# Kernel optimization log

Measured on AMD Instinct MI355X. Metric: run time of the kernel, lower is better.

The kernel has to match this reference:

```python
import jax, jax.numpy as jnp
import numpy as np

N_NODES = 10000
N_EDGES = 160000
HIDDEN = 256
HEADS = 8
LN_EPS = 1e-5


def setup_inputs() -> dict:
    key = jax.random.key(0)
    ks = jax.random.split(key, 8)
    s = 1.0 / np.sqrt(HIDDEN)
    return {
        "node_embeddings": jax.random.normal(ks[0], (1, N_NODES, HIDDEN), jnp.float32),
        "edge_index": jax.random.randint(ks[1], (2, N_EDGES), 0, N_NODES, dtype=jnp.int32),
        "Wq": jax.random.normal(ks[2], (HIDDEN, HIDDEN), jnp.float32) * s,
        "Wk": jax.random.normal(ks[3], (HIDDEN, HIDDEN), jnp.float32) * s,
        "Wv": jax.random.normal(ks[4], (HIDDEN, HIDDEN), jnp.float32) * s,
        "Wo": jax.random.normal(ks[5], (HIDDEN, HIDDEN), jnp.float32) * s,
        "ln_gamma": jnp.ones((HIDDEN,), jnp.float32),
        "ln_beta": jnp.zeros((HIDDEN,), jnp.float32),
    }


def reference(node_embeddings, edge_index, Wq, Wk, Wv, Wo, ln_gamma, ln_beta):
    B, N, Dm = node_embeddings.shape
    H = HEADS
    hd = Dm // H
    scale = 1.0 / np.sqrt(hd)

    def heads(x):  # [B,N,Dm] -> [B,H,N,hd]
        return x.reshape(B, N, H, hd).transpose(0, 2, 1, 3)

    Q = heads(node_embeddings @ Wq)
    K = heads(node_embeddings @ Wk)
    V = heads(node_embeddings @ Wv)

    src, dst = edge_index[0], edge_index[1]
    Qe = Q[:, :, src, :]           # [B,H,E,hd]
    Ke = K[:, :, dst, :]
    Ve = V[:, :, dst, :]

    scores = jnp.einsum('bhed,bhed->bhe', Qe, Ke) * scale   # [B,H,E]
    s_t = scores.transpose(2, 0, 1)                          # [E,B,H]
    smax = jax.ops.segment_max(s_t, src, num_segments=N)    # [N,B,H]
    ex = jnp.exp(s_t - smax[src])                            # [E,B,H]
    denom = jax.ops.segment_sum(ex, src, num_segments=N)    # [N,B,H]
    attn = ex / denom[src]                                   # scatter-softmax weights

    wV = attn[..., None] * Ve.transpose(2, 0, 1, 3)          # [E,B,H,hd]
    agg = jax.ops.segment_sum(wV, src, num_segments=N)      # [N,B,H,hd]
    attn_out = agg.transpose(1, 0, 2, 3).reshape(B, N, Dm)   # [B,N,Dm]

    out = attn_out @ Wo
    x = out + node_embeddings
    mu = jnp.mean(x, axis=-1, keepdims=True)
    var = jnp.mean((x - mu) ** 2, axis=-1, keepdims=True)
    return (x - mu) * jax.lax.rsqrt(var + LN_EPS) * ln_gamma + ln_beta
```

## Files before the change

kernel.cpp:

```cpp
#include <hip/hip_runtime.h>

#define NN 10000
#define NE 160000
#define DM 256
#define CAP 96
#define LN_EPSF 1e-5f
#define SCALEF 0.17677669529663687f

typedef unsigned short u16;
typedef __attribute__((ext_vector_type(4))) u16 u16x4;
typedef __attribute__((ext_vector_type(8))) u16 u16x8;
typedef __attribute__((ext_vector_type(4))) float f32x4;
typedef __attribute__((ext_vector_type(8))) short short8;

__device__ __forceinline__ float b2f(u16 u) { return __uint_as_float(((unsigned)u) << 16); }
__device__ __forceinline__ u16 f2b(float f) {
    unsigned u = __float_as_uint(f);
    return (u16)((u + 0x7fffu + ((u >> 16) & 1u)) >> 16);
}
__device__ __forceinline__ int clampi(int v) { return v < 0 ? 0 : (v >= NN ? NN - 1 : v); }

__global__ void k_fill_zero_f32(float* __restrict__ o, int n) {
    int i = blockIdx.x * 256 + threadIdx.x;
    if (i < n) o[i] = 0.f;
}

__global__ void k_prep(const float* __restrict__ Wq, const float* __restrict__ Wk,
                       const float* __restrict__ Wv, const float* __restrict__ Wo,
                       u16* __restrict__ Wt, int* __restrict__ cnt) {
    int id = blockIdx.x * 256 + threadIdx.x;
    if (id < NN) cnt[id] = 0;
    int m = id >> 16;
    int rc = id & 65535;
    int r = rc >> 8, c = rc & 255;
    const float* W = (m == 0) ? Wq : (m == 1) ? Wk : (m == 2) ? Wv : Wo;
    Wt[m * 65536 + c * 256 + r] = f2b(W[r * 256 + c]);
}

__global__ __launch_bounds__(256) void k_qkv_bucket(const float* __restrict__ X, const u16* __restrict__ Wt,
                                                    u16* __restrict__ Q, u16* __restrict__ KV,
                                                    const int* __restrict__ EI, int* __restrict__ cnt,
                                                    int* __restrict__ buck) {
    constexpr int AS = 40;
    __shared__ u16 At[64 * AS];
    __shared__ u16 Bt[256 * AS];
    if (blockIdx.y == 3) {
        int e = blockIdx.x * 256 + threadIdx.x;
        if (e < NE) {
            int s = clampi(EI[e]);
            int slot = atomicAdd(&cnt[s], 1);
            if (slot < CAP) buck[s * CAP + slot] = clampi(EI[NE + e]);
        }
        return;
    }
    if (blockIdx.x >= 157) return;
    const int t = threadIdx.x;
    const int w = t >> 6, l = t & 63, quad = l >> 4, m16 = l & 15;
    const int mat = blockIdx.y;
    const u16* Wm = Wt + mat * 65536;
    const int node0 = blockIdx.x * 64;
    f32x4 acc[4][4];
#pragma unroll
    for (int i = 0; i < 4; i++)
#pragma unroll
        for (int j = 0; j < 4; j++) acc[i][j] = (f32x4){0.f, 0.f, 0.f, 0.f};
    const int arow = t >> 2, ac8 = (t & 3) * 8;
    for (int k0 = 0; k0 < DM; k0 += 32) {
        u16x8 av = {0, 0, 0, 0, 0, 0, 0, 0};
        int anode = node0 + arow;
        if (anode < NN) {
            const float* xp = X + (size_t)anode * DM + k0 + ac8;
            f32x4 a0 = *(const f32x4*)(xp);
            f32x4 a1 = *(const f32x4*)(xp + 4);
            av[0] = f2b(a0[0]); av[1] = f2b(a0[1]); av[2] = f2b(a0[2]); av[3] = f2b(a0[3]);
            av[4] = f2b(a1[0]); av[5] = f2b(a1[1]); av[6] = f2b(a1[2]); av[7] = f2b(a1[3]);
        }
        *(u16x8*)(At + arow * AS + ac8) = av;
        const u16* bsrc = Wm + t * DM + k0;
        u16x8 b0 = *(const u16x8*)(bsrc);
        u16x8 b1 = *(const u16x8*)(bsrc + 8);
        u16x8 b2 = *(const u16x8*)(bsrc + 16);
        u16x8 b3 = *(const u16x8*)(bsrc + 24);
        u16* bd = Bt + t * AS;
        *(u16x8*)(bd) = b0;
        *(u16x8*)(bd + 8) = b1;
        *(u16x8*)(bd + 16) = b2;
        *(u16x8*)(bd + 24) = b3;
        __syncthreads();
        short8 a[4], b[4];
#pragma unroll
        for (int rt = 0; rt < 4; rt++)
            a[rt] = *(const short8*)(At + (rt * 16 + m16) * AS + quad * 8);
#pragma unroll
        for (int ct = 0; ct < 4; ct++)
            b[ct] = *(const short8*)(Bt + (w * 64 + ct * 16 + m16) * AS + quad * 8);
#pragma unroll
        for (int rt = 0; rt < 4; rt++)
#pragma unroll
            for (int ct = 0; ct < 4; ct++)
                acc[rt][ct] = __builtin_amdgcn_mfma_f32_16x16x32_bf16(a[rt], b[ct], acc[rt][ct], 0, 0, 0);
        __syncthreads();
    }
#pragma unroll
    for (int rt = 0; rt < 4; rt++) {
#pragma unroll
        for (int ct = 0; ct < 4; ct++) {
            int col = w * 64 + ct * 16 + m16;
#pragma unroll
            for (int r = 0; r < 4; r++) {
                int node = node0 + rt * 16 + quad * 4 + r;
                if (node < NN) {
                    u16 v = f2b(acc[rt][ct][r]);
                    if (mat == 0) Q[(size_t)node * DM + col] = v;
                    else KV[(size_t)node * 512 + (col >> 2) * 8 + (col & 3) + ((mat == 2) ? 4 : 0)] = v;
                }
            }
        }
    }
}

#define UPD(mm, ss, AA, kv, p) do {                  \
    float nm_ = fmaxf(mm, p);                        \
    float al_ = __expf(mm - nm_);                    \
    float pe_ = __expf(p - nm_);                     \
    ss = ss * al_ + pe_;                             \
    AA[0] = AA[0] * al_ + pe_ * b2f(kv[4]);          \
    AA[1] = AA[1] * al_ + pe_ * b2f(kv[5]);          \
    AA[2] = AA[2] * al_ + pe_ * b2f(kv[6]);          \
    AA[3] = AA[3] * al_ + pe_ * b2f(kv[7]);          \
    mm = nm_;                                        \
} while (0)

__global__ __launch_bounds__(256) void k_edge(const u16* __restrict__ Q, const u16* __restrict__ KV,
                                              const int* __restrict__ cnt, const int* __restrict__ buck,
                                              u16* __restrict__ attn) {
    const int t = threadIdx.x;
    const int w = t >> 6, l = t & 63;
    const int node = blockIdx.x * 4 + w;
    const int d0 = l * 4;
    int deg = cnt[node];
    if (deg > CAP) deg = CAP;
    const int* bl = buck + node * CAP;
    u16x4 q4 = *(const u16x4*)(Q + (size_t)node * DM + d0);
    float qf0 = b2f(q4[0]) * SCALEF, qf1 = b2f(q4[1]) * SCALEF;
    float qf2 = b2f(q4[2]) * SCALEF, qf3 = b2f(q4[3]) * SCALEF;
    float m0 = -3.0e38f, m1 = -3.0e38f, m2 = -3.0e38f, m3 = -3.0e38f;
    float s0 = 0.f, s1 = 0.f, s2 = 0.f, s3 = 0.f;
    f32x4 A0 = {0.f, 0.f, 0.f, 0.f}, A1 = {0.f, 0.f, 0.f, 0.f};
    f32x4 A2 = {0.f, 0.f, 0.f, 0.f}, A3 = {0.f, 0.f, 0.f, 0.f};
    int i = 0;
    int deg4 = deg & ~3;
    for (; i < deg4; i += 4) {
        int4 e4 = *(const int4*)(bl + i);
        u16x8 kv0 = *(const u16x8*)(KV + (size_t)e4.x * 512 + l * 8);
        u16x8 kv1 = *(const u16x8*)(KV + (size_t)e4.y * 512 + l * 8);
        u16x8 kv2 = *(const u16x8*)(KV + (size_t)e4.z * 512 + l * 8);
        u16x8 kv3 = *(const u16x8*)(KV + (size_t)e4.w * 512 + l * 8);
        float p0 = qf0 * b2f(kv0[0]) + qf1 * b2f(kv0[1]) + qf2 * b2f(kv0[2]) + qf3 * b2f(kv0[3]);
        float p1 = qf0 * b2f(kv1[0]) + qf1 * b2f(kv1[1]) + qf2 * b2f(kv1[2]) + qf3 * b2f(kv1[3]);
        float p2 = qf0 * b2f(kv2[0]) + qf1 * b2f(kv2[1]) + qf2 * b2f(kv2[2]) + qf3 * b2f(kv2[3]);
        float p3 = qf0 * b2f(kv3[0]) + qf1 * b2f(kv3[1]) + qf2 * b2f(kv3[2]) + qf3 * b2f(kv3[3]);
        p0 += __shfl_xor(p0, 1, 64); p1 += __shfl_xor(p1, 1, 64);
        p2 += __shfl_xor(p2, 1, 64); p3 += __shfl_xor(p3, 1, 64);
        p0 += __shfl_xor(p0, 2, 64); p1 += __shfl_xor(p1, 2, 64);
        p2 += __shfl_xor(p2, 2, 64); p3 += __shfl_xor(p3, 2, 64);
        p0 += __shfl_xor(p0, 4, 64); p1 += __shfl_xor(p1, 4, 64);
        p2 += __shfl_xor(p2, 4, 64); p3 += __shfl_xor(p3, 4, 64);
        UPD(m0, s0, A0, kv0, p0);
        UPD(m1, s1, A1, kv1, p1);
        UPD(m2, s2, A2, kv2, p2);
        UPD(m3, s3, A3, kv3, p3);
    }
    for (; i < deg; ++i) {
        int dst = bl[i];
        u16x8 kv = *(const u16x8*)(KV + (size_t)dst * 512 + l * 8);
        float p = qf0 * b2f(kv[0]) + qf1 * b2f(kv[1]) + qf2 * b2f(kv[2]) + qf3 * b2f(kv[3]);
        p += __shfl_xor(p, 1, 64);
        p += __shfl_xor(p, 2, 64);
        p += __shfl_xor(p, 4, 64);
        UPD(m0, s0, A0, kv, p);
    }
    float nm = fmaxf(fmaxf(m0, m1), fmaxf(m2, m3));
    float w0 = __expf(m0 - nm), w1 = __expf(m1 - nm);
    float w2 = __expf(m2 - nm), w3 = __expf(m3 - nm);
    float s = s0 * w0 + s1 * w1 + s2 * w2 + s3 * w3;
    float inv = (s > 0.f) ? 1.f / s : 0.f;
    u16x4 o;
    o[0] = f2b((A0[0] * w0 + A1[0] * w1 + A2[0] * w2 + A3[0] * w3) * inv);
    o[1] = f2b((A0[1] * w0 + A1[1] * w1 + A2[1] * w2 + A3[1] * w3) * inv);
    o[2] = f2b((A0[2] * w0 + A1[2] * w1 + A2[2] * w2 + A3[2] * w3) * inv);
    o[3] = f2b((A0[3] * w0 + A1[3] * w1 + A2[3] * w2 + A3[3] * w3) * inv);
    *(u16x4*)(attn + (size_t)node * DM + d0) = o;
}

__global__ __launch_bounds__(256) void k_gemm_out_ln(const u16* __restrict__ In, const u16* __restrict__ WoT,
                                                     const float* __restrict__ X, const float* __restrict__ g,
                                                     const float* __restrict__ b, float* __restrict__ out) {
    constexpr int AS = 40;
    __shared__ u16 At[64 * AS];
    __shared__ u16 Bt[256 * AS];
    __shared__ float gbuf[256], bbuf[256];
    __shared__ float redS[4][64], redQ[4][64];
    __shared__ float muS[64], rsS[64];
    const int t = threadIdx.x;
    gbuf[t] = g[t];
    bbuf[t] = b[t];
    const int w = t >> 6, l = t & 63, quad = l >> 4, m16 = l & 15;
    const int node0 = blockIdx.x * 64;
    f32x4 acc[4][4];
#pragma unroll
    for (int i = 0; i < 4; i++)
#pragma unroll
        for (int j = 0; j < 4; j++) acc[i][j] = (f32x4){0.f, 0.f, 0.f, 0.f};
    const int arow = t >> 2, ac8 = (t & 3) * 8;
    for (int k0 = 0; k0 < DM; k0 += 32) {
        u16x8 av = {0, 0, 0, 0, 0, 0, 0, 0};
        int anode = node0 + arow;
        if (anode < NN) av = *(const u16x8*)(In + (size_t)anode * DM + k0 + ac8);
        *(u16x8*)(At + arow * AS + ac8) = av;
        const u16* bsrc = WoT + t * DM + k0;
        u16x8 b0 = *(const u16x8*)(bsrc);
        u16x8 b1 = *(const u16x8*)(bsrc + 8);
        u16x8 b2 = *(const u16x8*)(bsrc + 16);
        u16x8 b3 = *(const u16x8*)(bsrc + 24);
        u16* bd = Bt + t * AS;
        *(u16x8*)(bd) = b0;
        *(u16x8*)(bd + 8) = b1;
        *(u16x8*)(bd + 16) = b2;
        *(u16x8*)(bd + 24) = b3;
        __syncthreads();
        short8 a[4], bf[4];
#pragma unroll
        for (int rt = 0; rt < 4; rt++)
            a[rt] = *(const short8*)(At + (rt * 16 + m16) * AS + quad * 8);
#pragma unroll
        for (int ct = 0; ct < 4; ct++)
            bf[ct] = *(const short8*)(Bt + (w * 64 + ct * 16 + m16) * AS + quad * 8);
#pragma unroll
        for (int rt = 0; rt < 4; rt++)
#pragma unroll
            for (int ct = 0; ct < 4; ct++)
                acc[rt][ct] = __builtin_amdgcn_mfma_f32_16x16x32_bf16(a[rt], bf[ct], acc[rt][ct], 0, 0, 0);
        __syncthreads();
    }
#pragma unroll
    for (int rt = 0; rt < 4; rt++)
#pragma unroll
        for (int ct = 0; ct < 4; ct++) {
            int col = w * 64 + ct * 16 + m16;
#pragma unroll
            for (int r = 0; r < 4; r++) {
                int node = node0 + rt * 16 + quad * 4 + r;
                float x = (node < NN) ? X[(size_t)node * DM + col] : 0.f;
                acc[rt][ct][r] += x;
            }
        }
#pragma unroll
    for (int rt = 0; rt < 4; rt++) {
#pragma unroll
        for (int r = 0; r < 4; r++) {
            float p1 = acc[rt][0][r] + acc[rt][1][r] + acc[rt][2][r] + acc[rt][3][r];
            float p2 = acc[rt][0][r] * acc[rt][0][r] + acc[rt][1][r] * acc[rt][1][r] +
                       acc[rt][2][r] * acc[rt][2][r] + acc[rt][3][r] * acc[rt][3][r];
#pragma unroll
            for (int o = 1; o < 16; o <<= 1) {
                p1 += __shfl_xor(p1, o, 64);
                p2 += __shfl_xor(p2, o, 64);
            }
            if (m16 == 0) {
                int row = rt * 16 + quad * 4 + r;
                redS[w][row] = p1;
                redQ[w][row] = p2;
            }
        }
    }
    __syncthreads();
    if (t < 64) {
        float s1t = redS[0][t] + redS[1][t] + redS[2][t] + redS[3][t];
        float s2t = redQ[0][t] + redQ[1][t] + redQ[2][t] + redQ[3][t];
        float mm = s1t * (1.f / DM);
        float var = s2t * (1.f / DM) - mm * mm;
        muS[t] = mm;
        rsS[t] = rsqrtf(var + LN_EPSF);
    }
    __syncthreads();
#pragma unroll
    for (int rt = 0; rt < 4; rt++)
#pragma unroll
        for (int ct = 0; ct < 4; ct++) {
            int col = w * 64 + ct * 16 + m16;
#pragma unroll
            for (int r = 0; r < 4; r++) {
                int row = rt * 16 + quad * 4 + r;
                int node = node0 + row;
                if (node < NN)
                    out[(size_t)node * DM + col] = (acc[rt][ct][r] - muS[row]) * rsS[row] * gbuf[col] + bbuf[col];
            }
        }
}

extern "C" void kernel_launch(void* const* d_in, const int* in_sizes, int n_in,
                              void* d_out, int out_size, void* d_ws, size_t ws_size,
                              hipStream_t stream) {
    (void)in_sizes; (void)n_in;
    const float* X  = (const float*)d_in[0];
    const int*   EI = (const int*)d_in[1];
    const float* Wq = (const float*)d_in[2];
    const float* Wk = (const float*)d_in[3];
    const float* Wv = (const float*)d_in[4];
    const float* Wo = (const float*)d_in[5];
    const float* g  = (const float*)d_in[6];
    const float* be = (const float*)d_in[7];

    const size_t SWT  = (size_t)4 * 65536 * 2;
    const size_t SKV  = (size_t)NN * 512 * 2;
    const size_t SAT  = (size_t)NN * DM * 2;
    const size_t SCNT = (size_t)NN * 4;
    const size_t SBK  = (size_t)NN * CAP * 4;
    const size_t need = SWT + SKV + SAT + SCNT + SBK;
    if (ws_size < need) {
        k_fill_zero_f32<<<(out_size + 255) / 256, 256, 0, stream>>>((float*)d_out, out_size);
        return;
    }
    char* p = (char*)d_ws;
    u16* Wt   = (u16*)p; p += SWT;
    u16* KVb  = (u16*)p; p += SKV;
    u16* attn = (u16*)p; p += SAT;
    int* cnt  = (int*)p; p += SCNT;
    int* buck = (int*)p; p += SBK;
    u16* Qb = (u16*)d_out;

    k_prep<<<1024, 256, 0, stream>>>(Wq, Wk, Wv, Wo, Wt, cnt);
    k_qkv_bucket<<<dim3(625, 4), 256, 0, stream>>>(X, Wt, Qb, KVb, EI, cnt, buck);
    k_edge<<<NN / 4, 256, 0, stream>>>(Qb, KVb, cnt, buck, attn);
    k_gemm_out_ln<<<157, 256, 0, stream>>>(attn, Wt + 3 * 65536, X, g, be, (float*)d_out);
}
```

Measured before the change: 143.7 us.

## Fuse all four stages into one cooperative persistent kernel with grid syncs

Replaces the four separate launches (weight prep, QKV GEMM plus edge bucketing, edge attention, output GEMM plus LayerNorm) with a single cooperative kernel of 512 blocks. Grid-wide syncs separate the phases, and each phase walks its work items in a grid-stride loop. The aim is to remove launch gaps and inter-kernel drain and fill. In exchange, the edge phase runs with fewer resident blocks, grid syncs cost time, and the output GEMM phase uses only 157 of 512 blocks. If the cooperative launch fails, the old four-kernel path runs instead.

```diff
diff --git a/kernel.cpp b/kernel.cpp
--- a/kernel.cpp
+++ b/kernel.cpp
@@ -1,4 +1,7 @@
 #include <hip/hip_runtime.h>
+#include <hip/hip_cooperative_groups.h>
+
+namespace cg = cooperative_groups;
 
 #define NN 10000
 #define NE 160000
@@ -6,6 +9,7 @@
 #define CAP 96
 #define LN_EPSF 1e-5f
 #define SCALEF 0.17677669529663687f
+#define GRIDB 512
 
 typedef unsigned short u16;
 typedef __attribute__((ext_vector_type(4))) u16 u16x4;
@@ -24,6 +28,18 @@
     int i = blockIdx.x * 256 + threadIdx.x;
     if (i < n) o[i] = 0.f;
 }
+
+#define UPD(mm, ss, AA, kv, p) do {                  \
+    float nm_ = fmaxf(mm, p);                        \
+    float al_ = __expf(mm - nm_);                    \
+    float pe_ = __expf(p - nm_);                     \
+    ss = ss * al_ + pe_;                             \
+    AA[0] = AA[0] * al_ + pe_ * b2f(kv[4]);          \
+    AA[1] = AA[1] * al_ + pe_ * b2f(kv[5]);          \
+    AA[2] = AA[2] * al_ + pe_ * b2f(kv[6]);          \
+    AA[3] = AA[3] * al_ + pe_ * b2f(kv[7]);          \
+    mm = nm_;                                        \
+} while (0)
 
 __global__ void k_prep(const float* __restrict__ Wq, const float* __restrict__ Wk,
                        const float* __restrict__ Wv, const float* __restrict__ Wo,
@@ -118,18 +134,6 @@
         }
     }
 }
-
-#define UPD(mm, ss, AA, kv, p) do {                  \
-    float nm_ = fmaxf(mm, p);                        \
-    float al_ = __expf(mm - nm_);                    \
-    float pe_ = __expf(p - nm_);                     \
-    ss = ss * al_ + pe_;                             \
-    AA[0] = AA[0] * al_ + pe_ * b2f(kv[4]);          \
-    AA[1] = AA[1] * al_ + pe_ * b2f(kv[5]);          \
-    AA[2] = AA[2] * al_ + pe_ * b2f(kv[6]);          \
-    AA[3] = AA[3] * al_ + pe_ * b2f(kv[7]);          \
-    mm = nm_;                                        \
-} while (0)
 
 __global__ __launch_bounds__(256) void k_edge(const u16* __restrict__ Q, const u16* __restrict__ KV,
                                               const int* __restrict__ cnt, const int* __restrict__ buck,
@@ -299,6 +303,272 @@
         }
 }
 
+__global__ __launch_bounds__(256, 2) void k_fused(
+    const float* __restrict__ X, const int* __restrict__ EI,
+    const float* __restrict__ Wq, const float* __restrict__ Wk,
+    const float* __restrict__ Wv, const float* __restrict__ Wo,
+    const float* __restrict__ g, const float* __restrict__ be,
+    float* out, u16* __restrict__ Wt, u16* __restrict__ KV,
+    u16* __restrict__ attn, int* __restrict__ cnt, int* __restrict__ buck,
+    u16* Q) {
+    constexpr int AS = 40;
+    __shared__ u16 At[64 * AS];
+    __shared__ u16 Bt[256 * AS];
+    __shared__ float gbuf[256], bbuf[256];
+    __shared__ float redS[4][64], redQ[4][64], muS[64], rsS[64];
+
+    const int t = threadIdx.x;
+    const int bid = blockIdx.x;
+    const int w = t >> 6, l = t & 63, quad = l >> 4, m16 = l & 15;
+    cg::grid_group gg = cg::this_grid();
+
+    for (int id = bid * 256 + t; id < 262144; id += GRIDB * 256) {
+        if (id < NN) cnt[id] = 0;
+        int m = id >> 16;
+        int rc = id & 65535;
+        int r = rc >> 8, c = rc & 255;
+        const float* W = (m == 0) ? Wq : (m == 1) ? Wk : (m == 2) ? Wv : Wo;
+        Wt[m * 65536 + c * 256 + r] = f2b(W[r * 256 + c]);
+    }
+    __threadfence();
+    gg.sync();
+
+    for (int item = bid; item < 1096; item += GRIDB) {
+        if (item >= 471) {
+            int e = (item - 471) * 256 + t;
+            if (e < NE) {
+                int s = clampi(EI[e]);
+                int slot = atomicAdd(&cnt[s], 1);
+                if (slot < CAP) buck[s * CAP + slot] = clampi(EI[NE + e]);
+            }
+            continue;
+        }
+        const int mat = item / 157;
+        const int tx = item % 157;
+        const u16* Wm = Wt + mat * 65536;
+        const int node0 = tx * 64;
+        f32x4 acc[4][4];
+#pragma unroll
+        for (int i = 0; i < 4; i++)
+#pragma unroll
+            for (int j = 0; j < 4; j++) acc[i][j] = (f32x4){0.f, 0.f, 0.f, 0.f};
+        const int arow = t >> 2, ac8 = (t & 3) * 8;
+        for (int k0 = 0; k0 < DM; k0 += 32) {
+            u16x8 av = {0, 0, 0, 0, 0, 0, 0, 0};
+            int anode = node0 + arow;
+            if (anode < NN) {
+                const float* xp = X + (size_t)anode * DM + k0 + ac8;
+                f32x4 a0 = *(const f32x4*)(xp);
+                f32x4 a1 = *(const f32x4*)(xp + 4);
+                av[0] = f2b(a0[0]); av[1] = f2b(a0[1]); av[2] = f2b(a0[2]); av[3] = f2b(a0[3]);
+                av[4] = f2b(a1[0]); av[5] = f2b(a1[1]); av[6] = f2b(a1[2]); av[7] = f2b(a1[3]);
+            }
+            *(u16x8*)(At + arow * AS + ac8) = av;
+            const u16* bsrc = Wm + t * DM + k0;
+            u16x8 b0 = *(const u16x8*)(bsrc);
+            u16x8 b1 = *(const u16x8*)(bsrc + 8);
+            u16x8 b2 = *(const u16x8*)(bsrc + 16);
+            u16x8 b3 = *(const u16x8*)(bsrc + 24);
+            u16* bd = Bt + t * AS;
+            *(u16x8*)(bd) = b0;
+            *(u16x8*)(bd + 8) = b1;
+            *(u16x8*)(bd + 16) = b2;
+            *(u16x8*)(bd + 24) = b3;
+            __syncthreads();
+            short8 a[4], b[4];
+#pragma unroll
+            for (int rt = 0; rt < 4; rt++)
+                a[rt] = *(const short8*)(At + (rt * 16 + m16) * AS + quad * 8);
+#pragma unroll
+            for (int ct = 0; ct < 4; ct++)
+                b[ct] = *(const short8*)(Bt + (w * 64 + ct * 16 + m16) * AS + quad * 8);
+#pragma unroll
+            for (int rt = 0; rt < 4; rt++)
+#pragma unroll
+                for (int ct = 0; ct < 4; ct++)
+                    acc[rt][ct] = __builtin_amdgcn_mfma_f32_16x16x32_bf16(a[rt], b[ct], acc[rt][ct], 0, 0, 0);
+            __syncthreads();
+        }
+#pragma unroll
+        for (int rt = 0; rt < 4; rt++) {
+#pragma unroll
+            for (int ct = 0; ct < 4; ct++) {
+                int col = w * 64 + ct * 16 + m16;
+#pragma unroll
+                for (int r = 0; r < 4; r++) {
+                    int node = node0 + rt * 16 + quad * 4 + r;
+                    if (node < NN) {
+                        u16 v = f2b(acc[rt][ct][r]);
+                        if (mat == 0) Q[(size_t)node * DM + col] = v;
+                        else KV[(size_t)node * 512 + (col >> 2) * 8 + (col & 3) + ((mat == 2) ? 4 : 0)] = v;
+                    }
+                }
+            }
+        }
+    }
+    __threadfence();
+    gg.sync();
+
+    {
+        const int d0 = l * 4;
+        for (int it = bid; it < 2500; it += GRIDB) {
+            const int node = it * 4 + w;
+            int deg = cnt[node];
+            if (deg > CAP) deg = CAP;
+            const int* bl = buck + node * CAP;
+            u16x4 q4 = *(const u16x4*)(Q + (size_t)node * DM + d0);
+            float qf0 = b2f(q4[0]) * SCALEF, qf1 = b2f(q4[1]) * SCALEF;
+            float qf2 = b2f(q4[2]) * SCALEF, qf3 = b2f(q4[3]) * SCALEF;
+            float m0 = -3.0e38f, m1 = -3.0e38f, m2 = -3.0e38f, m3 = -3.0e38f;
+            float s0 = 0.f, s1 = 0.f, s2 = 0.f, s3 = 0.f;
+            f32x4 A0 = {0.f, 0.f, 0.f, 0.f}, A1 = {0.f, 0.f, 0.f, 0.f};
+            f32x4 A2 = {0.f, 0.f, 0.f, 0.f}, A3 = {0.f, 0.f, 0.f, 0.f};
+            int i = 0;
+            int deg4 = deg & ~3;
+            for (; i < deg4; i += 4) {
+                int4 e4 = *(const int4*)(bl + i);
+                u16x8 kv0 = *(const u16x8*)(KV + (size_t)e4.x * 512 + l * 8);
+                u16x8 kv1 = *(const u16x8*)(KV + (size_t)e4.y * 512 + l * 8);
+                u16x8 kv2 = *(const u16x8*)(KV + (size_t)e4.z * 512 + l * 8);
+                u16x8 kv3 = *(const u16x8*)(KV + (size_t)e4.w * 512 + l * 8);
+                float p0 = qf0 * b2f(kv0[0]) + qf1 * b2f(kv0[1]) + qf2 * b2f(kv0[2]) + qf3 * b2f(kv0[3]);
+                float p1 = qf0 * b2f(kv1[0]) + qf1 * b2f(kv1[1]) + qf2 * b2f(kv1[2]) + qf3 * b2f(kv1[3]);
+                float p2 = qf0 * b2f(kv2[0]) + qf1 * b2f(kv2[1]) + qf2 * b2f(kv2[2]) + qf3 * b2f(kv2[3]);
+                float p3 = qf0 * b2f(kv3[0]) + qf1 * b2f(kv3[1]) + qf2 * b2f(kv3[2]) + qf3 * b2f(kv3[3]);
+                p0 += __shfl_xor(p0, 1, 64); p1 += __shfl_xor(p1, 1, 64);
+                p2 += __shfl_xor(p2, 1, 64); p3 += __shfl_xor(p3, 1, 64);
+                p0 += __shfl_xor(p0, 2, 64); p1 += __shfl_xor(p1, 2, 64);
+                p2 += __shfl_xor(p2, 2, 64); p3 += __shfl_xor(p3, 2, 64);
+                p0 += __shfl_xor(p0, 4, 64); p1 += __shfl_xor(p1, 4, 64);
+                p2 += __shfl_xor(p2, 4, 64); p3 += __shfl_xor(p3, 4, 64);
+                UPD(m0, s0, A0, kv0, p0);
+                UPD(m1, s1, A1, kv1, p1);
+                UPD(m2, s2, A2, kv2, p2);
+                UPD(m3, s3, A3, kv3, p3);
+            }
+            for (; i < deg; ++i) {
+                int dst = bl[i];
+                u16x8 kv = *(const u16x8*)(KV + (size_t)dst * 512 + l * 8);
+                float p = qf0 * b2f(kv[0]) + qf1 * b2f(kv[1]) + qf2 * b2f(kv[2]) + qf3 * b2f(kv[3]);
+                p += __shfl_xor(p, 1, 64);
+                p += __shfl_xor(p, 2, 64);
+                p += __shfl_xor(p, 4, 64);
+                UPD(m0, s0, A0, kv, p);
+            }
+            float nm = fmaxf(fmaxf(m0, m1), fmaxf(m2, m3));
+            float w0 = __expf(m0 - nm), w1 = __expf(m1 - nm);
+            float w2 = __expf(m2 - nm), w3 = __expf(m3 - nm);
+            float S = s0 * w0 + s1 * w1 + s2 * w2 + s3 * w3;
+            float inv = (S > 0.f) ? 1.f / S : 0.f;
+            u16x4 o;
+            o[0] = f2b((A0[0] * w0 + A1[0] * w1 + A2[0] * w2 + A3[0] * w3) * inv);
+            o[1] = f2b((A0[1] * w0 + A1[1] * w1 + A2[1] * w2 + A3[1] * w3) * inv);
+            o[2] = f2b((A0[2] * w0 + A1[2] * w1 + A2[2] * w2 + A3[2] * w3) * inv);
+            o[3] = f2b((A0[3] * w0 + A1[3] * w1 + A2[3] * w2 + A3[3] * w3) * inv);
+            *(u16x4*)(attn + (size_t)node * DM + d0) = o;
+        }
+    }
+    __threadfence();
+    gg.sync();
+
+    for (int it = bid; it < 157; it += GRIDB) {
+        const u16* WoT = Wt + 3 * 65536;
+        gbuf[t] = g[t];
+        bbuf[t] = be[t];
+        const int node0 = it * 64;
+        f32x4 acc[4][4];
+#pragma unroll
+        for (int i = 0; i < 4; i++)
+#pragma unroll
+            for (int j = 0; j < 4; j++) acc[i][j] = (f32x4){0.f, 0.f, 0.f, 0.f};
+        const int arow = t >> 2, ac8 = (t & 3) * 8;
+        for (int k0 = 0; k0 < DM; k0 += 32) {
+            u16x8 av = {0, 0, 0, 0, 0, 0, 0, 0};
+            int anode = node0 + arow;
+            if (anode < NN) av = *(const u16x8*)(attn + (size_t)anode * DM + k0 + ac8);
+            *(u16x8*)(At + arow * AS + ac8) = av;
+            const u16* bsrc = WoT + t * DM + k0;
+            u16x8 b0 = *(const u16x8*)(bsrc);
+            u16x8 b1 = *(const u16x8*)(bsrc + 8);
+            u16x8 b2 = *(const u16x8*)(bsrc + 16);
+            u16x8 b3 = *(const u16x8*)(bsrc + 24);
+            u16* bd = Bt + t * AS;
+            *(u16x8*)(bd) = b0;
+            *(u16x8*)(bd + 8) = b1;
+            *(u16x8*)(bd + 16) = b2;
+            *(u16x8*)(bd + 24) = b3;
+            __syncthreads();
+            short8 a[4], bf[4];
+#pragma unroll
+            for (int rt = 0; rt < 4; rt++)
+                a[rt] = *(const short8*)(At + (rt * 16 + m16) * AS + quad * 8);
+#pragma unroll
+            for (int ct = 0; ct < 4; ct++)
+                bf[ct] = *(const short8*)(Bt + (w * 64 + ct * 16 + m16) * AS + quad * 8);
+#pragma unroll
+            for (int rt = 0; rt < 4; rt++)
+#pragma unroll
+                for (int ct = 0; ct < 4; ct++)
+                    acc[rt][ct] = __builtin_amdgcn_mfma_f32_16x16x32_bf16(a[rt], bf[ct], acc[rt][ct], 0, 0, 0);
+            __syncthreads();
+        }
+#pragma unroll
+        for (int rt = 0; rt < 4; rt++)
+#pragma unroll
+            for (int ct = 0; ct < 4; ct++) {
+                int col = w * 64 + ct * 16 + m16;
+#pragma unroll
+                for (int r = 0; r < 4; r++) {
+                    int node = node0 + rt * 16 + quad * 4 + r;
+                    float x = (node < NN) ? X[(size_t)node * DM + col] : 0.f;
+                    acc[rt][ct][r] += x;
+                }
+            }
+#pragma unroll
+        for (int rt = 0; rt < 4; rt++) {
+#pragma unroll
+            for (int r = 0; r < 4; r++) {
+                float p1 = acc[rt][0][r] + acc[rt][1][r] + acc[rt][2][r] + acc[rt][3][r];
+                float p2 = acc[rt][0][r] * acc[rt][0][r] + acc[rt][1][r] * acc[rt][1][r] +
+                           acc[rt][2][r] * acc[rt][2][r] + acc[rt][3][r] * acc[rt][3][r];
+#pragma unroll
+                for (int o = 1; o < 16; o <<= 1) {
+                    p1 += __shfl_xor(p1, o, 64);
+                    p2 += __shfl_xor(p2, o, 64);
+                }
+                if (m16 == 0) {
+                    int row = rt * 16 + quad * 4 + r;
+                    redS[w][row] = p1;
+                    redQ[w][row] = p2;
+                }
+            }
+        }
+        __syncthreads();
+        if (t < 64) {
+            float s1t = redS[0][t] + redS[1][t] + redS[2][t] + redS[3][t];
+            float s2t = redQ[0][t] + redQ[1][t] + redQ[2][t] + redQ[3][t];
+            float mm = s1t * (1.f / DM);
+            float var = s2t * (1.f / DM) - mm * mm;
+            muS[t] = mm;
+            rsS[t] = rsqrtf(var + LN_EPSF);
+        }
+        __syncthreads();
+#pragma unroll
+        for (int rt = 0; rt < 4; rt++)
+#pragma unroll
+            for (int ct = 0; ct < 4; ct++) {
+                int col = w * 64 + ct * 16 + m16;
+#pragma unroll
+                for (int r = 0; r < 4; r++) {
+                    int row = rt * 16 + quad * 4 + r;
+                    int node = node0 + row;
+                    if (node < NN)
+                        out[(size_t)node * DM + col] = (acc[rt][ct][r] - muS[row]) * rsS[row] * gbuf[col] + bbuf[col];
+                }
+            }
+    }
+}
+
 extern "C" void kernel_launch(void* const* d_in, const int* in_sizes, int n_in,
                               void* d_out, int out_size, void* d_ws, size_t ws_size,
                               hipStream_t stream) {
@@ -317,6 +587,7 @@
     const size_t SAT  = (size_t)NN * DM * 2;
     const size_t SCNT = (size_t)NN * 4;
     const size_t SBK  = (size_t)NN * CAP * 4;
+    const size_t SQB  = (size_t)NN * DM * 2;
     const size_t need = SWT + SKV + SAT + SCNT + SBK;
     if (ws_size < need) {
         k_fill_zero_f32<<<(out_size + 255) / 256, 256, 0, stream>>>((float*)d_out, out_size);
@@ -328,10 +599,18 @@
     u16* attn = (u16*)p; p += SAT;
     int* cnt  = (int*)p; p += SCNT;
     int* buck = (int*)p; p += SBK;
-    u16* Qb = (u16*)d_out;
-
-    k_prep<<<1024, 256, 0, stream>>>(Wq, Wk, Wv, Wo, Wt, cnt);
-    k_qkv_bucket<<<dim3(625, 4), 256, 0, stream>>>(X, Wt, Qb, KVb, EI, cnt, buck);
-    k_edge<<<NN / 4, 256, 0, stream>>>(Qb, KVb, cnt, buck, attn);
-    k_gemm_out_ln<<<157, 256, 0, stream>>>(attn, Wt + 3 * 65536, X, g, be, (float*)d_out);
-}
+    u16* Qb = (ws_size >= need + SQB) ? (u16*)p : (u16*)d_out;
+    float* outp = (float*)d_out;
+
+    void* args[] = {(void*)&X, (void*)&EI, (void*)&Wq, (void*)&Wk, (void*)&Wv, (void*)&Wo,
+                    (void*)&g, (void*)&be, (void*)&outp, (void*)&Wt, (void*)&KVb, (void*)&attn,
+                    (void*)&cnt, (void*)&buck, (void*)&Qb};
+    hipError_t err = hipLaunchCooperativeKernel((void*)k_fused, dim3(GRIDB), dim3(256), args, 0, stream);
+    if (err != hipSuccess) {
+        (void)hipGetLastError();
+        k_prep<<<1024, 256, 0, stream>>>(Wq, Wk, Wv, Wo, Wt, cnt);
+        k_qkv_bucket<<<dim3(625, 4), 256, 0, stream>>>(X, Wt, Qb, KVb, EI, cnt, buck);
+        k_edge<<<NN / 4, 256, 0, stream>>>(Qb, KVb, cnt, buck, attn);
+        k_gemm_out_ln<<<157, 256, 0, stream>>>(attn, Wt + 3 * 65536, X, g, be, (float*)d_out);
+    }
+}
```

New measurement: 486.0 us. 3.38x slower.

## Fuse edge attention with output GEMM+LayerNorm and share X tile across QKV

Applied to the files above, without the earlier changes.

The edge softmax-aggregation kernel is merged with the output projection and LayerNorm. Each block handles 16 nodes, keeps the aggregated attention rows in shared memory, and runs the Wo MFMA GEMM directly, so the bf16 attention buffer no longer makes a global round trip. The QKV kernel now loads the converted X tile once into shared memory and loops over the three weight matrices, with the grid shrinking from 4 to 2 y-slices. Exchanges: fewer, longer-running blocks in the QKV GEMM (157 instead of 471), and a smaller 16-row GEMM per block in the fused kernel that reloads the whole Wo matrix per block.

```diff
diff --git a/kernel.cpp b/kernel.cpp
--- a/kernel.cpp
+++ b/kernel.cpp
@@ -23,100 +23,6 @@
 __global__ void k_fill_zero_f32(float* __restrict__ o, int n) {
     int i = blockIdx.x * 256 + threadIdx.x;
     if (i < n) o[i] = 0.f;
-}
-
-__global__ void k_prep(const float* __restrict__ Wq, const float* __restrict__ Wk,
-                       const float* __restrict__ Wv, const float* __restrict__ Wo,
-                       u16* __restrict__ Wt, int* __restrict__ cnt) {
-    int id = blockIdx.x * 256 + threadIdx.x;
-    if (id < NN) cnt[id] = 0;
-    int m = id >> 16;
-    int rc = id & 65535;
-    int r = rc >> 8, c = rc & 255;
-    const float* W = (m == 0) ? Wq : (m == 1) ? Wk : (m == 2) ? Wv : Wo;
-    Wt[m * 65536 + c * 256 + r] = f2b(W[r * 256 + c]);
-}
-
-__global__ __launch_bounds__(256) void k_qkv_bucket(const float* __restrict__ X, const u16* __restrict__ Wt,
-                                                    u16* __restrict__ Q, u16* __restrict__ KV,
-                                                    const int* __restrict__ EI, int* __restrict__ cnt,
-                                                    int* __restrict__ buck) {
-    constexpr int AS = 40;
-    __shared__ u16 At[64 * AS];
-    __shared__ u16 Bt[256 * AS];
-    if (blockIdx.y == 3) {
-        int e = blockIdx.x * 256 + threadIdx.x;
-        if (e < NE) {
-            int s = clampi(EI[e]);
-            int slot = atomicAdd(&cnt[s], 1);
-            if (slot < CAP) buck[s * CAP + slot] = clampi(EI[NE + e]);
-        }
-        return;
-    }
-    if (blockIdx.x >= 157) return;
-    const int t = threadIdx.x;
-    const int w = t >> 6, l = t & 63, quad = l >> 4, m16 = l & 15;
-    const int mat = blockIdx.y;
-    const u16* Wm = Wt + mat * 65536;
-    const int node0 = blockIdx.x * 64;
-    f32x4 acc[4][4];
-#pragma unroll
-    for (int i = 0; i < 4; i++)
-#pragma unroll
-        for (int j = 0; j < 4; j++) acc[i][j] = (f32x4){0.f, 0.f, 0.f, 0.f};
-    const int arow = t >> 2, ac8 = (t & 3) * 8;
-    for (int k0 = 0; k0 < DM; k0 += 32) {
-        u16x8 av = {0, 0, 0, 0, 0, 0, 0, 0};
-        int anode = node0 + arow;
-        if (anode < NN) {
-            const float* xp = X + (size_t)anode * DM + k0 + ac8;
-            f32x4 a0 = *(const f32x4*)(xp);
-            f32x4 a1 = *(const f32x4*)(xp + 4);
-            av[0] = f2b(a0[0]); av[1] = f2b(a0[1]); av[2] = f2b(a0[2]); av[3] = f2b(a0[3]);
-            av[4] = f2b(a1[0]); av[5] = f2b(a1[1]); av[6] = f2b(a1[2]); av[7] = f2b(a1[3]);
-        }
-        *(u16x8*)(At + arow * AS + ac8) = av;
-        const u16* bsrc = Wm + t * DM + k0;
-        u16x8 b0 = *(const u16x8*)(bsrc);
-        u16x8 b1 = *(const u16x8*)(bsrc + 8);
-        u16x8 b2 = *(const u16x8*)(bsrc + 16);
-        u16x8 b3 = *(const u16x8*)(bsrc + 24);
-        u16* bd = Bt + t * AS;
-        *(u16x8*)(bd) = b0;
-        *(u16x8*)(bd + 8) = b1;
-        *(u16x8*)(bd + 16) = b2;
-        *(u16x8*)(bd + 24) = b3;
-        __syncthreads();
-        short8 a[4], b[4];
-#pragma unroll
-        for (int rt = 0; rt < 4; rt++)
-            a[rt] = *(const short8*)(At + (rt * 16 + m16) * AS + quad * 8);
-#pragma unroll
-        for (int ct = 0; ct < 4; ct++)
-            b[ct] = *(const short8*)(Bt + (w * 64 + ct * 16 + m16) * AS + quad * 8);
-#pragma unroll
-        for (int rt = 0; rt < 4; rt++)
-#pragma unroll
-            for (int ct = 0; ct < 4; ct++)
-                acc[rt][ct] = __builtin_amdgcn_mfma_f32_16x16x32_bf16(a[rt], b[ct], acc[rt][ct], 0, 0, 0);
-        __syncthreads();
-    }
-#pragma unroll
-    for (int rt = 0; rt < 4; rt++) {
-#pragma unroll
-        for (int ct = 0; ct < 4; ct++) {
-            int col = w * 64 + ct * 16 + m16;
-#pragma unroll
-            for (int r = 0; r < 4; r++) {
-                int node = node0 + rt * 16 + quad * 4 + r;
-                if (node < NN) {
-                    u16 v = f2b(acc[rt][ct][r]);
-                    if (mat == 0) Q[(size_t)node * DM + col] = v;
-                    else KV[(size_t)node * 512 + (col >> 2) * 8 + (col & 3) + ((mat == 2) ? 4 : 0)] = v;
-                }
-            }
-        }
-    }
 }
 
 #define UPD(mm, ss, AA, kv, p) do {                  \
@@ -131,151 +37,230 @@
     mm = nm_;                                        \
 } while (0)
 
-__global__ __launch_bounds__(256) void k_edge(const u16* __restrict__ Q, const u16* __restrict__ KV,
-                                              const int* __restrict__ cnt, const int* __restrict__ buck,
-                                              u16* __restrict__ attn) {
+__global__ void k_prep(const float* __restrict__ Wq, const float* __restrict__ Wk,
+                       const float* __restrict__ Wv, const float* __restrict__ Wo,
+                       u16* __restrict__ Wt, int* __restrict__ cnt) {
+    int id = blockIdx.x * 256 + threadIdx.x;
+    if (id < NN) cnt[id] = 0;
+    int m = id >> 16;
+    int rc = id & 65535;
+    int r = rc >> 8, c = rc & 255;
+    const float* W = (m == 0) ? Wq : (m == 1) ? Wk : (m == 2) ? Wv : Wo;
+    Wt[m * 65536 + c * 256 + r] = f2b(W[r * 256 + c]);
+}
+
+__global__ __launch_bounds__(256) void k_qkv_bucket(const float* __restrict__ X, const u16* __restrict__ Wt,
+                                                    u16* __restrict__ Q, u16* __restrict__ KV,
+                                                    const int* __restrict__ EI, int* __restrict__ cnt,
+                                                    int* __restrict__ buck) {
+    constexpr int BS = 40;
+    constexpr int ASF = 264;
+    __shared__ u16 At[64 * ASF];
+    __shared__ u16 Bt[256 * BS];
+    if (blockIdx.y == 1) {
+        int e = blockIdx.x * 256 + threadIdx.x;
+        if (e < NE) {
+            int s = clampi(EI[e]);
+            int slot = atomicAdd(&cnt[s], 1);
+            if (slot < CAP) buck[s * CAP + slot] = clampi(EI[NE + e]);
+        }
+        return;
+    }
+    if (blockIdx.x >= 157) return;
     const int t = threadIdx.x;
-    const int w = t >> 6, l = t & 63;
-    const int node = blockIdx.x * 4 + w;
-    const int d0 = l * 4;
-    int deg = cnt[node];
-    if (deg > CAP) deg = CAP;
-    const int* bl = buck + node * CAP;
-    u16x4 q4 = *(const u16x4*)(Q + (size_t)node * DM + d0);
-    float qf0 = b2f(q4[0]) * SCALEF, qf1 = b2f(q4[1]) * SCALEF;
-    float qf2 = b2f(q4[2]) * SCALEF, qf3 = b2f(q4[3]) * SCALEF;
-    float m0 = -3.0e38f, m1 = -3.0e38f, m2 = -3.0e38f, m3 = -3.0e38f;
-    float s0 = 0.f, s1 = 0.f, s2 = 0.f, s3 = 0.f;
-    f32x4 A0 = {0.f, 0.f, 0.f, 0.f}, A1 = {0.f, 0.f, 0.f, 0.f};
-    f32x4 A2 = {0.f, 0.f, 0.f, 0.f}, A3 = {0.f, 0.f, 0.f, 0.f};
-    int i = 0;
-    int deg4 = deg & ~3;
-    for (; i < deg4; i += 4) {
-        int4 e4 = *(const int4*)(bl + i);
-        u16x8 kv0 = *(const u16x8*)(KV + (size_t)e4.x * 512 + l * 8);
-        u16x8 kv1 = *(const u16x8*)(KV + (size_t)e4.y * 512 + l * 8);
-        u16x8 kv2 = *(const u16x8*)(KV + (size_t)e4.z * 512 + l * 8);
-        u16x8 kv3 = *(const u16x8*)(KV + (size_t)e4.w * 512 + l * 8);
-        float p0 = qf0 * b2f(kv0[0]) + qf1 * b2f(kv0[1]) + qf2 * b2f(kv0[2]) + qf3 * b2f(kv0[3]);
-        float p1 = qf0 * b2f(kv1[0]) + qf1 * b2f(kv1[1]) + qf2 * b2f(kv1[2]) + qf3 * b2f(kv1[3]);
-        float p2 = qf0 * b2f(kv2[0]) + qf1 * b2f(kv2[1]) + qf2 * b2f(kv2[2]) + qf3 * b2f(kv2[3]);
-        float p3 = qf0 * b2f(kv3[0]) + qf1 * b2f(kv3[1]) + qf2 * b2f(kv3[2]) + qf3 * b2f(kv3[3]);
-        p0 += __shfl_xor(p0, 1, 64); p1 += __shfl_xor(p1, 1, 64);
-        p2 += __shfl_xor(p2, 1, 64); p3 += __shfl_xor(p3, 1, 64);
-        p0 += __shfl_xor(p0, 2, 64); p1 += __shfl_xor(p1, 2, 64);
-        p2 += __shfl_xor(p2, 2, 64); p3 += __shfl_xor(p3, 2, 64);
-        p0 += __shfl_xor(p0, 4, 64); p1 += __shfl_xor(p1, 4, 64);
-        p2 += __shfl_xor(p2, 4, 64); p3 += __shfl_xor(p3, 4, 64);
-        UPD(m0, s0, A0, kv0, p0);
-        UPD(m1, s1, A1, kv1, p1);
-        UPD(m2, s2, A2, kv2, p2);
-        UPD(m3, s3, A3, kv3, p3);
-    }
-    for (; i < deg; ++i) {
-        int dst = bl[i];
-        u16x8 kv = *(const u16x8*)(KV + (size_t)dst * 512 + l * 8);
-        float p = qf0 * b2f(kv[0]) + qf1 * b2f(kv[1]) + qf2 * b2f(kv[2]) + qf3 * b2f(kv[3]);
-        p += __shfl_xor(p, 1, 64);
-        p += __shfl_xor(p, 2, 64);
-        p += __shfl_xor(p, 4, 64);
-        UPD(m0, s0, A0, kv, p);
-    }
-    float nm = fmaxf(fmaxf(m0, m1), fmaxf(m2, m3));
-    float w0 = __expf(m0 - nm), w1 = __expf(m1 - nm);
-    float w2 = __expf(m2 - nm), w3 = __expf(m3 - nm);
-    float s = s0 * w0 + s1 * w1 + s2 * w2 + s3 * w3;
-    float inv = (s > 0.f) ? 1.f / s : 0.f;
-    u16x4 o;
-    o[0] = f2b((A0[0] * w0 + A1[0] * w1 + A2[0] * w2 + A3[0] * w3) * inv);
-    o[1] = f2b((A0[1] * w0 + A1[1] * w1 + A2[1] * w2 + A3[1] * w3) * inv);
-    o[2] = f2b((A0[2] * w0 + A1[2] * w1 + A2[2] * w2 + A3[2] * w3) * inv);
-    o[3] = f2b((A0[3] * w0 + A1[3] * w1 + A2[3] * w2 + A3[3] * w3) * inv);
-    *(u16x4*)(attn + (size_t)node * DM + d0) = o;
-}
-
-__global__ __launch_bounds__(256) void k_gemm_out_ln(const u16* __restrict__ In, const u16* __restrict__ WoT,
-                                                     const float* __restrict__ X, const float* __restrict__ g,
-                                                     const float* __restrict__ b, float* __restrict__ out) {
-    constexpr int AS = 40;
-    __shared__ u16 At[64 * AS];
-    __shared__ u16 Bt[256 * AS];
+    const int w = t >> 6, l = t & 63, quad = l >> 4, m16 = l & 15;
+    const int node0 = blockIdx.x * 64;
+    const int arow = t >> 2, ac8 = (t & 3) * 8;
+    const int anode = node0 + arow;
+#pragma unroll
+    for (int k0 = 0; k0 < DM; k0 += 32) {
+        u16x8 av = {0, 0, 0, 0, 0, 0, 0, 0};
+        if (anode < NN) {
+            const float* xp = X + (size_t)anode * DM + k0 + ac8;
+            f32x4 a0 = *(const f32x4*)(xp);
+            f32x4 a1 = *(const f32x4*)(xp + 4);
+            av[0] = f2b(a0[0]); av[1] = f2b(a0[1]); av[2] = f2b(a0[2]); av[3] = f2b(a0[3]);
+            av[4] = f2b(a1[0]); av[5] = f2b(a1[1]); av[6] = f2b(a1[2]); av[7] = f2b(a1[3]);
+        }
+        *(u16x8*)(At + arow * ASF + k0 + ac8) = av;
+    }
+    __syncthreads();
+    for (int mat = 0; mat < 3; mat++) {
+        const u16* Wm = Wt + mat * 65536;
+        f32x4 acc[4][4];
+#pragma unroll
+        for (int i = 0; i < 4; i++)
+#pragma unroll
+            for (int j = 0; j < 4; j++) acc[i][j] = (f32x4){0.f, 0.f, 0.f, 0.f};
+        for (int k0 = 0; k0 < DM; k0 += 32) {
+            const u16* bsrc = Wm + t * DM + k0;
+            u16x8 b0 = *(const u16x8*)(bsrc);
+            u16x8 b1 = *(const u16x8*)(bsrc + 8);
+            u16x8 b2 = *(const u16x8*)(bsrc + 16);
+            u16x8 b3 = *(const u16x8*)(bsrc + 24);
+            u16* bd = Bt + t * BS;
+            *(u16x8*)(bd) = b0;
+            *(u16x8*)(bd + 8) = b1;
+            *(u16x8*)(bd + 16) = b2;
+            *(u16x8*)(bd + 24) = b3;
+            __syncthreads();
+            short8 a[4], b[4];
+#pragma unroll
+            for (int rt = 0; rt < 4; rt++)
+                a[rt] = *(const short8*)(At + (rt * 16 + m16) * ASF + k0 + quad * 8);
+#pragma unroll
+            for (int ct = 0; ct < 4; ct++)
+                b[ct] = *(const short8*)(Bt + (w * 64 + ct * 16 + m16) * BS + quad * 8);
+#pragma unroll
+            for (int rt = 0; rt < 4; rt++)
+#pragma unroll
+                for (int ct = 0; ct < 4; ct++)
+                    acc[rt][ct] = __builtin_amdgcn_mfma_f32_16x16x32_bf16(a[rt], b[ct], acc[rt][ct], 0, 0, 0);
+            __syncthreads();
+        }
+#pragma unroll
+        for (int rt = 0; rt < 4; rt++) {
+#pragma unroll
+            for (int ct = 0; ct < 4; ct++) {
+                int col = w * 64 + ct * 16 + m16;
+#pragma unroll
+                for (int r = 0; r < 4; r++) {
+                    int node = node0 + rt * 16 + quad * 4 + r;
+                    if (node < NN) {
+                        u16 v = f2b(acc[rt][ct][r]);
+                        if (mat == 0) Q[(size_t)node * DM + col] = v;
+                        else KV[(size_t)node * 512 + (col >> 2) * 8 + (col & 3) + ((mat == 2) ? 4 : 0)] = v;
+                    }
+                }
+            }
+        }
+    }
+}
+
+__global__ __launch_bounds__(256) void k_edge_out_ln(const u16* __restrict__ Q, const u16* __restrict__ KV,
+                                                     const int* __restrict__ cnt, const int* __restrict__ buck,
+                                                     const u16* __restrict__ WoT, const float* __restrict__ X,
+                                                     const float* __restrict__ g, const float* __restrict__ b,
+                                                     float* __restrict__ out) {
+    constexpr int BS = 40;
+    constexpr int ALS = 264;
+    __shared__ u16 AtL[16 * ALS];
+    __shared__ u16 Bt[256 * BS];
     __shared__ float gbuf[256], bbuf[256];
-    __shared__ float redS[4][64], redQ[4][64];
-    __shared__ float muS[64], rsS[64];
+    __shared__ float redS[4][16], redQ[4][16], muS[16], rsS[16];
     const int t = threadIdx.x;
+    const int w = t >> 6, l = t & 63, quad = l >> 4, m16 = l & 15;
+    const int nodeB = blockIdx.x * 16;
     gbuf[t] = g[t];
     bbuf[t] = b[t];
-    const int w = t >> 6, l = t & 63, quad = l >> 4, m16 = l & 15;
-    const int node0 = blockIdx.x * 64;
-    f32x4 acc[4][4];
-#pragma unroll
-    for (int i = 0; i < 4; i++)
-#pragma unroll
-        for (int j = 0; j < 4; j++) acc[i][j] = (f32x4){0.f, 0.f, 0.f, 0.f};
-    const int arow = t >> 2, ac8 = (t & 3) * 8;
+    const int d0 = l * 4;
+    for (int nl = w; nl < 16; nl += 4) {
+        const int node = nodeB + nl;
+        int deg = cnt[node];
+        if (deg > CAP) deg = CAP;
+        const int* bl = buck + node * CAP;
+        u16x4 q4 = *(const u16x4*)(Q + (size_t)node * DM + d0);
+        float qf0 = b2f(q4[0]) * SCALEF, qf1 = b2f(q4[1]) * SCALEF;
+        float qf2 = b2f(q4[2]) * SCALEF, qf3 = b2f(q4[3]) * SCALEF;
+        float m0 = -3.0e38f, m1 = -3.0e38f, m2 = -3.0e38f, m3 = -3.0e38f;
+        float s0 = 0.f, s1 = 0.f, s2 = 0.f, s3 = 0.f;
+        f32x4 A0 = {0.f, 0.f, 0.f, 0.f}, A1 = {0.f, 0.f, 0.f, 0.f};
+        f32x4 A2 = {0.f, 0.f, 0.f, 0.f}, A3 = {0.f, 0.f, 0.f, 0.f};
+        int i = 0;
+        int deg4 = deg & ~3;
+        for (; i < deg4; i += 4) {
+            int4 e4 = *(const int4*)(bl + i);
+            u16x8 kv0 = *(const u16x8*)(KV + (size_t)e4.x * 512 + l * 8);
+            u16x8 kv1 = *(const u16x8*)(KV + (size_t)e4.y * 512 + l * 8);
+            u16x8 kv2 = *(const u16x8*)(KV + (size_t)e4.z * 512 + l * 8);
+            u16x8 kv3 = *(const u16x8*)(KV + (size_t)e4.w * 512 + l * 8);
+            float p0 = qf0 * b2f(kv0[0]) + qf1 * b2f(kv0[1]) + qf2 * b2f(kv0[2]) + qf3 * b2f(kv0[3]);
+            float p1 = qf0 * b2f(kv1[0]) + qf1 * b2f(kv1[1]) + qf2 * b2f(kv1[2]) + qf3 * b2f(kv1[3]);
+            float p2 = qf0 * b2f(kv2[0]) + qf1 * b2f(kv2[1]) + qf2 * b2f(kv2[2]) + qf3 * b2f(kv2[3]);
+            float p3 = qf0 * b2f(kv3[0]) + qf1 * b2f(kv3[1]) + qf2 * b2f(kv3[2]) + qf3 * b2f(kv3[3]);
+            p0 += __shfl_xor(p0, 1, 64); p1 += __shfl_xor(p1, 1, 64);
+            p2 += __shfl_xor(p2, 1, 64); p3 += __shfl_xor(p3, 1, 64);
+            p0 += __shfl_xor(p0, 2, 64); p1 += __shfl_xor(p1, 2, 64);
+            p2 += __shfl_xor(p2, 2, 64); p3 += __shfl_xor(p3, 2, 64);
+            p0 += __shfl_xor(p0, 4, 64); p1 += __shfl_xor(p1, 4, 64);
+            p2 += __shfl_xor(p2, 4, 64); p3 += __shfl_xor(p3, 4, 64);
+            UPD(m0, s0, A0, kv0, p0);
+            UPD(m1, s1, A1, kv1, p1);
+            UPD(m2, s2, A2, kv2, p2);
+            UPD(m3, s3, A3, kv3, p3);
+        }
+        for (; i < deg; ++i) {
+            int dst = bl[i];
+            u16x8 kv = *(const u16x8*)(KV + (size_t)dst * 512 + l * 8);
+            float p = qf0 * b2f(kv[0]) + qf1 * b2f(kv[1]) + qf2 * b2f(kv[2]) + qf3 * b2f(kv[3]);
+            p += __shfl_xor(p, 1, 64);
+            p += __shfl_xor(p, 2, 64);
+            p += __shfl_xor(p, 4, 64);
+            UPD(m0, s0, A0, kv, p);
+        }
+        float nm = fmaxf(fmaxf(m0, m1), fmaxf(m2, m3));
+        float w0 = __expf(m0 - nm), w1 = __expf(m1 - nm);
+        float w2 = __expf(m2 - nm), w3 = __expf(m3 - nm);
+        float S = s0 * w0 + s1 * w1 + s2 * w2 + s3 * w3;
+        float inv = (S > 0.f) ? 1.f / S : 0.f;
+        u16x4 o;
+        o[0] = f2b((A0[0] * w0 + A1[0] * w1 + A2[0] * w2 + A3[0] * w3) * inv);
+        o[1] = f2b((A0[1] * w0 + A1[1] * w1 + A2[1] * w2 + A3[1] * w3) * inv);
+        o[2] = f2b((A0[2] * w0 + A1[2] * w1 + A2[2] * w2 + A3[2] * w3) * inv);
+        o[3] = f2b((A0[3] * w0 + A1[3] * w1 + A2[3] * w2 + A3[3] * w3) * inv);
+        *(u16x4*)(AtL + nl * ALS + d0) = o;
+    }
+    __syncthreads();
+    f32x4 acc[4];
+#pragma unroll
+    for (int ct = 0; ct < 4; ct++) acc[ct] = (f32x4){0.f, 0.f, 0.f, 0.f};
     for (int k0 = 0; k0 < DM; k0 += 32) {
-        u16x8 av = {0, 0, 0, 0, 0, 0, 0, 0};
-        int anode = node0 + arow;
-        if (anode < NN) av = *(const u16x8*)(In + (size_t)anode * DM + k0 + ac8);
-        *(u16x8*)(At + arow * AS + ac8) = av;
         const u16* bsrc = WoT + t * DM + k0;
         u16x8 b0 = *(const u16x8*)(bsrc);
         u16x8 b1 = *(const u16x8*)(bsrc + 8);
         u16x8 b2 = *(const u16x8*)(bsrc + 16);
         u16x8 b3 = *(const u16x8*)(bsrc + 24);
-        u16* bd = Bt + t * AS;
+        u16* bd = Bt + t * BS;
         *(u16x8*)(bd) = b0;
         *(u16x8*)(bd + 8) = b1;
         *(u16x8*)(bd + 16) = b2;
         *(u16x8*)(bd + 24) = b3;
         __syncthreads();
-        short8 a[4], bf[4];
-#pragma unroll
-        for (int rt = 0; rt < 4; rt++)
-            a[rt] = *(const short8*)(At + (rt * 16 + m16) * AS + quad * 8);
-#pragma unroll
-        for (int ct = 0; ct < 4; ct++)
-            bf[ct] = *(const short8*)(Bt + (w * 64 + ct * 16 + m16) * AS + quad * 8);
-#pragma unroll
-        for (int rt = 0; rt < 4; rt++)
-#pragma unroll
-            for (int ct = 0; ct < 4; ct++)
-                acc[rt][ct] = __builtin_amdgcn_mfma_f32_16x16x32_bf16(a[rt], bf[ct], acc[rt][ct], 0, 0, 0);
+        short8 a = *(const short8*)(AtL + m16 * ALS + k0 + quad * 8);
+#pragma unroll
+        for (int ct = 0; ct < 4; ct++) {
+            short8 bf = *(const short8*)(Bt + (w * 64 + ct * 16 + m16) * BS + quad * 8);
+            acc[ct] = __builtin_amdgcn_mfma_f32_16x16x32_bf16(a, bf, acc[ct], 0, 0, 0);
+        }
         __syncthreads();
     }
-#pragma unroll
-    for (int rt = 0; rt < 4; rt++)
-#pragma unroll
-        for (int ct = 0; ct < 4; ct++) {
-            int col = w * 64 + ct * 16 + m16;
-#pragma unroll
-            for (int r = 0; r < 4; r++) {
-                int node = node0 + rt * 16 + quad * 4 + r;
-                float x = (node < NN) ? X[(size_t)node * DM + col] : 0.f;
-                acc[rt][ct][r] += x;
-            }
-        }
-#pragma unroll
-    for (int rt = 0; rt < 4; rt++) {
+    float val[4][4];
+#pragma unroll
+    for (int ct = 0; ct < 4; ct++) {
+        int col = w * 64 + ct * 16 + m16;
 #pragma unroll
         for (int r = 0; r < 4; r++) {
-            float p1 = acc[rt][0][r] + acc[rt][1][r] + acc[rt][2][r] + acc[rt][3][r];
-            float p2 = acc[rt][0][r] * acc[rt][0][r] + acc[rt][1][r] * acc[rt][1][r] +
-                       acc[rt][2][r] * acc[rt][2][r] + acc[rt][3][r] * acc[rt][3][r];
-#pragma unroll
-            for (int o = 1; o < 16; o <<= 1) {
-                p1 += __shfl_xor(p1, o, 64);
-                p2 += __shfl_xor(p2, o, 64);
-            }
-            if (m16 == 0) {
-                int row = rt * 16 + quad * 4 + r;
-                redS[w][row] = p1;
-                redQ[w][row] = p2;
-            }
+            int row = quad * 4 + r;
+            val[ct][r] = acc[ct][r] + X[(size_t)(nodeB + row) * DM + col];
+        }
+    }
+#pragma unroll
+    for (int r = 0; r < 4; r++) {
+        float p1 = val[0][r] + val[1][r] + val[2][r] + val[3][r];
+        float p2 = val[0][r] * val[0][r] + val[1][r] * val[1][r] +
+                   val[2][r] * val[2][r] + val[3][r] * val[3][r];
+#pragma unroll
+        for (int o = 1; o < 16; o <<= 1) {
+            p1 += __shfl_xor(p1, o, 64);
+            p2 += __shfl_xor(p2, o, 64);
+        }
+        if (m16 == 0) {
+            redS[w][quad * 4 + r] = p1;
+            redQ[w][quad * 4 + r] = p2;
         }
     }
     __syncthreads();
-    if (t < 64) {
+    if (t < 16) {
         float s1t = redS[0][t] + redS[1][t] + redS[2][t] + redS[3][t];
         float s2t = redQ[0][t] + redQ[1][t] + redQ[2][t] + redQ[3][t];
         float mm = s1t * (1.f / DM);
@@ -285,18 +270,14 @@
     }
     __syncthreads();
 #pragma unroll
-    for (int rt = 0; rt < 4; rt++)
-#pragma unroll
-        for (int ct = 0; ct < 4; ct++) {
-            int col = w * 64 + ct * 16 + m16;
-#pragma unroll
-            for (int r = 0; r < 4; r++) {
-                int row = rt * 16 + quad * 4 + r;
-                int node = node0 + row;
-                if (node < NN)
-                    out[(size_t)node * DM + col] = (acc[rt][ct][r] - muS[row]) * rsS[row] * gbuf[col] + bbuf[col];
-            }
-        }
+    for (int ct = 0; ct < 4; ct++) {
+        int col = w * 64 + ct * 16 + m16;
+#pragma unroll
+        for (int r = 0; r < 4; r++) {
+            int row = quad * 4 + r;
+            out[(size_t)(nodeB + row) * DM + col] = (val[ct][r] - muS[row]) * rsS[row] * gbuf[col] + bbuf[col];
+        }
+    }
 }
 
 extern "C" void kernel_launch(void* const* d_in, const int* in_sizes, int n_in,
@@ -314,10 +295,10 @@
 
     const size_t SWT  = (size_t)4 * 65536 * 2;
     const size_t SKV  = (size_t)NN * 512 * 2;
-    const size_t SAT  = (size_t)NN * DM * 2;
     const size_t SCNT = (size_t)NN * 4;
     const size_t SBK  = (size_t)NN * CAP * 4;
-    const size_t need = SWT + SKV + SAT + SCNT + SBK;
+    const size_t SQB  = (size_t)NN * DM * 2;
+    const size_t need = SWT + SKV + SCNT + SBK + SQB;
     if (ws_size < need) {
         k_fill_zero_f32<<<(out_size + 255) / 256, 256, 0, stream>>>((float*)d_out, out_size);
         return;
@@ -325,13 +306,11 @@
     char* p = (char*)d_ws;
     u16* Wt   = (u16*)p; p += SWT;
     u16* KVb  = (u16*)p; p += SKV;
-    u16* attn = (u16*)p; p += SAT;
     int* cnt  = (int*)p; p += SCNT;
     int* buck = (int*)p; p += SBK;
-    u16* Qb = (u16*)d_out;
+    u16* Qb   = (u16*)p; p += SQB;
 
     k_prep<<<1024, 256, 0, stream>>>(Wq, Wk, Wv, Wo, Wt, cnt);
-    k_qkv_bucket<<<dim3(625, 4), 256, 0, stream>>>(X, Wt, Qb, KVb, EI, cnt, buck);
-    k_edge<<<NN / 4, 256, 0, stream>>>(Qb, KVb, cnt, buck, attn);
-    k_gemm_out_ln<<<157, 256, 0, stream>>>(attn, Wt + 3 * 65536, X, g, be, (float*)d_out);
-}
+    k_qkv_bucket<<<dim3(625, 2), 256, 0, stream>>>(X, Wt, Qb, KVb, EI, cnt, buck);
+    k_edge_out_ln<<<625, 256, 0, stream>>>(Qb, KVb, cnt, buck, Wt + 3 * 65536, X, g, be, (float*)d_out);
+}
```

New measurement: 148.3 us. 3.2% more time.
